# Kernel tuning notes

Hardware: AMD Instinct MI355X
Metric: run time of the kernel (lower is better)

## Reference

```python
import jax, jax.numpy as jnp
import numpy as np

B, M, D, H, DH = 8, 1024, 768, 12, 64
R, RF, RW, DFF = 32, 384, 384, 3072
EPS = 1e-12  # BERT LayerNorm eps


def _ln(z, g, b):
    mu = jnp.mean(z, -1, keepdims=True)
    var = jnp.mean((z - mu) ** 2, -1, keepdims=True)
    return g * (z - mu) * jax.lax.rsqrt(var + EPS) + b


def setup_inputs() -> dict:
    ks = jax.random.split(jax.random.key(0), 20)
    n = lambda k, s: jax.random.normal(k, s, dtype=jnp.float32) * 0.02
    return {
        "x": jax.random.normal(ks[0], (B, M, D), dtype=jnp.float32),
        "mask": jnp.zeros((B, M), jnp.float32),  # additive attention mask
        "Pq": n(ks[1], (H, D, R)), "Vq": n(ks[2], (H, R, DH)), "bq": n(ks[3], (H, DH)),
        "Pk": n(ks[4], (H, D, R)), "Vk": n(ks[5], (H, R, DH)), "bk": n(ks[6], (H, DH)),
        "Pv": n(ks[7], (H, D, R)), "Vv": n(ks[8], (H, R, DH)), "bv": n(ks[9], (H, DH)),
        "Uo": n(ks[10], (D, RW)), "Vo": n(ks[11], (RW, D)), "bo_attn": n(ks[12], (D,)),
        "U1": n(ks[13], (D, RF)), "V1": n(ks[14], (RF, DFF)), "b1": n(ks[15], (DFF,)),
        "U2": n(ks[16], (DFF, RF)), "V2": n(ks[17], (RF, D)), "b2": n(ks[18], (D,)),
        "ln1_g": jnp.ones((D,), jnp.float32), "ln1_b": jnp.zeros((D,), jnp.float32),
        "ln2_g": jnp.ones((D,), jnp.float32), "ln2_b": jnp.zeros((D,), jnp.float32),
    }


def reference(x, mask, Pq, Vq, bq, Pk, Vk, bk, Pv, Vv, bv, Uo, Vo, bo_attn,
              U1, V1, b1, U2, V2, b2, ln1_g, ln1_b, ln2_g, ln2_b):
    Bx, Mx, dm = x.shape
    dh = dm // Pq.shape[0]
    scale = 1.0 / (dh ** 0.5)
    # low-rank per-head Q/K/V: x @ P (d->r) then @ V (r->dh), + per-head bias
    Q = jnp.einsum('bmd,hdr,hrk->bhmk', x, Pq, Vq) + bq[None, :, None, :]
    K = jnp.einsum('bmd,hdr,hrk->bhmk', x, Pk, Vk) + bk[None, :, None, :]
    V = jnp.einsum('bmd,hdr,hrk->bhmk', x, Pv, Vv) + bv[None, :, None, :]
    scores = jnp.einsum('bhmk,bhnk->bhmn', Q, K) * scale + mask[:, None, None, :]
    probs = jax.nn.softmax(scores, axis=-1)
    attn = jnp.einsum('bhmn,bhnk->bhmk', probs, V)
    attn = attn.transpose(0, 2, 1, 3).reshape(Bx, Mx, dm)  # (B, M, d_model)
    # low-rank attention output projection + residual + LN1
    x1 = _ln(x + (attn @ Uo) @ Vo + bo_attn, ln1_g, ln1_b)
    # low-rank FFN: GELU((x1 @ U1) @ V1 + b1) @ U2 @ V2 + b2 (BERT exact gelu)
    mid = x1 @ U1
    y = (jax.nn.gelu(mid @ V1 + b1, approximate=False) @ U2) @ V2 + b2
    return _ln(x1 + y, ln2_g, ln2_b)
```

## Files before the change

### kernel.cpp

```cpp
#include <hip/hip_runtime.h>
#include <cstddef>

#define D_MODEL 768
#define NHEAD   12
#define DHEAD   64
#define RANK    32
#define SEQ     1024
#define BATCH   8
#define BM      8192

typedef __attribute__((ext_vector_type(8))) short short8;
typedef __attribute__((ext_vector_type(4))) float floatx4;

__device__ inline ushort f2b(float f) {
  union { float f; unsigned u; } v; v.f = f;
  unsigned r = v.u + 0x7fffu + ((v.u >> 16) & 1u);
  return (ushort)(r >> 16);
}
__device__ inline float b2f(ushort h) {
  union { unsigned u; float f; } v; v.u = ((unsigned)h) << 16;
  return v.f;
}
__device__ inline unsigned pk2(float a, float b) {
  return ((__float_as_uint(b) + 0x8000u) & 0xffff0000u) |
         ((__float_as_uint(a) + 0x8000u) >> 16);
}
__device__ inline float fast_gelu(float x) {
  float z = 0.79788456080286536f * (x + 0.044715f * x * x * x);
  float e = __expf(2.f * z);
  float t = 1.f - 2.f / (e + 1.f);
  return 0.5f * x * (1.f + t);
}

__global__ __launch_bounds__(256) void f2b_kernel(
    const float* __restrict__ in, ushort* __restrict__ out, int n) {
  int i = (blockIdx.x * 256 + threadIdx.x) * 4;
  if (i >= n) return;
  float4 v = *(const float4*)(in + i);
  ushort4 o;
  o.x = f2b(v.x); o.y = f2b(v.y); o.z = f2b(v.z); o.w = f2b(v.w);
  *(ushort4*)(out + i) = o;
}

__global__ __launch_bounds__(256) void combine_qkv_kernel(
    const float* __restrict__ Pq, const float* __restrict__ Vq,
    const float* __restrict__ Pk, const float* __restrict__ Vk,
    const float* __restrict__ Pv, const float* __restrict__ Vv,
    ushort* __restrict__ Wt) {
  int which = blockIdx.y;
  const float* P  = which == 0 ? Pq : (which == 1 ? Pk : Pv);
  const float* Vw = which == 0 ? Vq : (which == 1 ? Vk : Vv);
  ushort* W = Wt + (size_t)which * D_MODEL * D_MODEL;
  int idx = blockIdx.x * 256 + threadIdx.x;
  if (idx >= D_MODEL * NHEAD * DHEAD) return;
  int c = idx / D_MODEL;
  int d = idx - c * D_MODEL;
  int h = c >> 6, k = c & 63;
  const float* p = P + ((size_t)h * D_MODEL + d) * RANK;
  const float* v = Vw + (size_t)h * RANK * DHEAD + k;
  float s = 0.f;
#pragma unroll
  for (int r = 0; r < RANK; r++) s += p[r] * v[(size_t)r * DHEAD];
  W[(size_t)c * D_MODEL + d] = f2b(s);
}

__global__ __launch_bounds__(256) void concat_bias_kernel(
    const float* __restrict__ bq, const float* __restrict__ bk,
    const float* __restrict__ bv, float* __restrict__ out) {
  int i = blockIdx.x * 256 + threadIdx.x;
  if (i >= 2304) return;
  out[i] = (i < 768) ? bq[i] : (i < 1536 ? bk[i - 768] : bv[i - 1536]);
}

__global__ __launch_bounds__(256) void prep_weights_kernel(
    const float* __restrict__ U1, const float* __restrict__ V1,
    const float* __restrict__ U2, const float* __restrict__ V2,
    const float* __restrict__ Vo, const float* __restrict__ Uo,
    ushort* __restrict__ U1t, ushort* __restrict__ V1t,
    ushort* __restrict__ U2t, ushort* __restrict__ V2t,
    ushort* __restrict__ VoT, ushort* __restrict__ Uob) {
  __shared__ float t[32][33];
  int blk = blockIdx.x;
  if (blk >= 3168) {
    int i = (blk - 3168) * 1024 + threadIdx.x * 4;
    float4 v = *(const float4*)(Uo + i);
    ushort4 o;
    o.x = f2b(v.x); o.y = f2b(v.y); o.z = f2b(v.z); o.w = f2b(v.w);
    *(ushort4*)(Uob + i) = o;
    return;
  }
  const float* in; ushort* out; int R, C, bx, by;
  if (blk < 288)       { in = U1; out = U1t; R = 768;  C = 384;  int i = blk;        bx = i % 12; by = i / 12; }
  else if (blk < 1440) { in = V1; out = V1t; R = 384;  C = 3072; int i = blk - 288;  bx = i % 96; by = i / 96; }
  else if (blk < 2592) { in = U2; out = U2t; R = 3072; C = 384;  int i = blk - 1440; bx = i % 12; by = i / 12; }
  else if (blk < 2880) { in = V2; out = V2t; R = 384;  C = 768;  int i = blk - 2592; bx = i % 24; by = i / 24; }
  else                 { in = Vo; out = VoT; R = 384;  C = 768;  int i = blk - 2880; bx = i % 24; by = i / 24; }
  int c0 = bx * 32, r0 = by * 32;
  int lx = threadIdx.x & 31, ly = threadIdx.x >> 5;
#pragma unroll
  for (int i = 0; i < 32; i += 8)
    t[ly + i][lx] = in[(size_t)(r0 + ly + i) * C + c0 + lx];
  __syncthreads();
#pragma unroll
  for (int i = 0; i < 32; i += 8)
    out[(size_t)(c0 + ly + i) * R + r0 + lx] = f2b(t[lx][ly + i]);
}

template <int OUTMODE, int BIAS, int GELU>
__global__ __launch_bounds__(256, 2) void gemm_mfma_kernel(
    const ushort* __restrict__ A, const ushort* __restrict__ Bt,
    const float* __restrict__ bias, void* __restrict__ C,
    void* __restrict__ C2, void* __restrict__ C3,
    int M, int N, int K) {
  __shared__ __align__(16) ushort Als[2][128 * 64];
  __shared__ __align__(16) ushort Bls[2][128 * 64];
  const int tid  = threadIdx.x;
  const int lane = tid & 63;
  const int quad = lane >> 4, l16 = lane & 15;
  const int wu   = __builtin_amdgcn_readfirstlane(tid >> 6);
  const int wrow = (wu >> 1) * 64, wcol = (wu & 1) * 64;
  const int row0 = blockIdx.x * 128, col0 = blockIdx.y * 128;

  const int r_ = tid >> 3, sl_ = tid & 7;
  const ushort* Ag = A + (size_t)(row0 + r_) * K + sl_ * 8;
  const ushort* Bg = Bt + (size_t)(col0 + r_) * K + sl_ * 8;
  const int loff = r_ * 64 + ((sl_ ^ (r_ & 7)) << 3);

  const int nsteps = K >> 6;
  short8 ast[4], bst[4];

#pragma unroll
  for (int p = 0; p < 4; p++) {
    ast[p] = *(const short8*)(Ag + (size_t)(32 * p) * K);
    bst[p] = *(const short8*)(Bg + (size_t)(32 * p) * K);
  }
#pragma unroll
  for (int p = 0; p < 4; p++) {
    *(short8*)(&Als[0][0] + loff + p * (32 * 64)) = ast[p];
    *(short8*)(&Bls[0][0] + loff + p * (32 * 64)) = bst[p];
  }
#pragma unroll
  for (int p = 0; p < 4; p++) {
    ast[p] = *(const short8*)(Ag + (size_t)(32 * p) * K + 64);
    bst[p] = *(const short8*)(Bg + (size_t)(32 * p) * K + 64);
  }
  asm volatile("s_waitcnt lgkmcnt(0)" ::: "memory");
  __builtin_amdgcn_s_barrier();
  asm volatile("" ::: "memory");

  floatx4 acc[4][4] = {};

  for (int s = 0; s < nsteps; s++) {
    const int cur = s & 1;

    if (s + 1 < nsteps) {
#pragma unroll
      for (int p = 0; p < 4; p++) {
        *(short8*)(&Als[cur ^ 1][0] + loff + p * (32 * 64)) = ast[p];
        *(short8*)(&Bls[cur ^ 1][0] + loff + p * (32 * 64)) = bst[p];
      }
      if (s + 2 < nsteps) {
        const int ko = (s + 2) * 64;
#pragma unroll
        for (int p = 0; p < 4; p++) {
          ast[p] = *(const short8*)(Ag + (size_t)(32 * p) * K + ko);
          bst[p] = *(const short8*)(Bg + (size_t)(32 * p) * K + ko);
        }
      }
    }

    __builtin_amdgcn_s_setprio(1);
#pragma unroll
    for (int kk = 0; kk < 2; kk++) {
      short8 af[4], bf[4];
#pragma unroll
      for (int mt = 0; mt < 4; mt++) {
        int row = wrow + mt * 16 + l16;
        af[mt] = *(const short8*)(&Als[cur][0] + row * 64
                                  + (((kk * 4 + quad) ^ (l16 & 7)) << 3));
      }
#pragma unroll
      for (int nt = 0; nt < 4; nt++) {
        int row = wcol + nt * 16 + l16;
        bf[nt] = *(const short8*)(&Bls[cur][0] + row * 64
                                  + (((kk * 4 + quad) ^ (l16 & 7)) << 3));
      }
#pragma unroll
      for (int mt = 0; mt < 4; mt++)
#pragma unroll
        for (int nt = 0; nt < 4; nt++)
          acc[mt][nt] = __builtin_amdgcn_mfma_f32_16x16x32_bf16(
              af[mt], bf[nt], acc[mt][nt], 0, 0, 0);
    }
    __builtin_amdgcn_s_setprio(0);

    if (s + 1 < nsteps) {
      asm volatile("s_waitcnt lgkmcnt(0)" ::: "memory");
      __builtin_amdgcn_s_barrier();
      asm volatile("" ::: "memory");
    }
  }

#pragma unroll
  for (int mt = 0; mt < 4; mt++) {
#pragma unroll
    for (int nt = 0; nt < 4; nt++) {
      int colg = col0 + wcol + nt * 16 + l16;
      float bv_ = BIAS ? bias[colg] : 0.f;
      float v4[4];
#pragma unroll
      for (int r = 0; r < 4; r++) {
        float v = acc[mt][nt][r] + bv_;
        if (GELU) v = fast_gelu(v);
        v4[r] = v;
      }
      int rowg0 = row0 + wrow + mt * 16 + quad * 4;
      if (OUTMODE == 3) {
        int seg = col0 / 768;
        int cl = colg - seg * 768;
        if (seg == 2) {
          ushort4 o;
          o.x = f2b(v4[0]); o.y = f2b(v4[1]); o.z = f2b(v4[2]); o.w = f2b(v4[3]);
          *(ushort4*)((ushort*)C3 + (size_t)cl * BM + rowg0) = o;
        } else {
          ushort* dst = (seg == 0) ? (ushort*)C : (ushort*)C2;
          float sc = (seg == 0) ? 0.125f : 1.f;
#pragma unroll
          for (int r = 0; r < 4; r++)
            dst[(size_t)(rowg0 + r) * D_MODEL + cl] = f2b(v4[r] * sc);
        }
      } else {
#pragma unroll
        for (int r = 0; r < 4; r++)
          ((ushort*)C)[(size_t)(rowg0 + r) * N + colg] = f2b(v4[r]);
      }
    }
  }
}

template <int BIAS>
__global__ __launch_bounds__(256) void gemm_n64_kernel(
    const ushort* __restrict__ A, const ushort* __restrict__ Bt,
    const float* __restrict__ bias, ushort* __restrict__ C,
    int M, int N, int K) {
  __shared__ __align__(16) ushort Als[128 * 32];
  __shared__ __align__(16) ushort Bls[64 * 32];
  const int tid  = threadIdx.x;
  const int lane = tid & 63;
  const int quad = lane >> 4, l16 = lane & 15;
  const int wu   = __builtin_amdgcn_readfirstlane(tid >> 6);
  const int row0 = blockIdx.x * 128, col0 = blockIdx.y * 64;

  floatx4 acc[2][4] = {};

  for (int k0 = 0; k0 < K; k0 += 32) {
    __syncthreads();
#pragma unroll
    for (int is = 0; is < 2; is++) {
      int c = is * 256 + wu * 64 + lane;
      int m = c >> 2, kk = (c & 3) << 3;
      const ushort* ga = A + (size_t)(row0 + m) * K + (k0 + kk);
      ushort* la = Als + (size_t)(is * 256 + wu * 64) * 8;
      __builtin_amdgcn_global_load_lds(
          (const __attribute__((address_space(1))) void*)ga,
          (__attribute__((address_space(3))) void*)la, 16, 0, 0);
    }
    {
      int c = wu * 64 + lane;
      int m = c >> 2, kk = (c & 3) << 3;
      const ushort* gb = Bt + (size_t)(col0 + m) * K + (k0 + kk);
      ushort* lb = Bls + (size_t)(wu * 64) * 8;
      __builtin_amdgcn_global_load_lds(
          (const __attribute__((address_space(1))) void*)gb,
          (__attribute__((address_space(3))) void*)lb, 16, 0, 0);
    }
    __syncthreads();

    short8 af[2], bf[4];
#pragma unroll
    for (int mt = 0; mt < 2; mt++)
      af[mt] = *(const short8*)(Als + ((wu * 32 + mt * 16 + l16) * 32 + quad * 8));
#pragma unroll
    for (int nt = 0; nt < 4; nt++)
      bf[nt] = *(const short8*)(Bls + ((nt * 16 + l16) * 32 + quad * 8));
#pragma unroll
    for (int mt = 0; mt < 2; mt++)
#pragma unroll
      for (int nt = 0; nt < 4; nt++)
        acc[mt][nt] = __builtin_amdgcn_mfma_f32_16x16x32_bf16(
            af[mt], bf[nt], acc[mt][nt], 0, 0, 0);
  }

#pragma unroll
  for (int mt = 0; mt < 2; mt++) {
#pragma unroll
    for (int nt = 0; nt < 4; nt++) {
      int colg = col0 + nt * 16 + l16;
      float bv_ = BIAS ? bias[colg] : 0.f;
      int rowg0 = row0 + wu * 32 + mt * 16 + quad * 4;
#pragma unroll
      for (int r = 0; r < 4; r++)
        C[(size_t)(rowg0 + r) * N + colg] = f2b(acc[mt][nt][r] + bv_);
    }
  }
}

__global__ __launch_bounds__(256) void gemm_mfma_splitk_kernel(
    const ushort* __restrict__ A, const ushort* __restrict__ Bt,
    float* __restrict__ Cpart, int M, int N, int Ktot, int Kper) {
  __shared__ __align__(16) ushort Als[128 * 32];
  __shared__ __align__(16) ushort Bls[128 * 32];
  const int tid  = threadIdx.x;
  const int lane = tid & 63;
  const int quad = lane >> 4, l16 = lane & 15;
  const int wu   = __builtin_amdgcn_readfirstlane(tid >> 6);
  const int wrow = (wu >> 1) * 64, wcol = (wu & 1) * 64;
  const int row0 = blockIdx.x * 128, col0 = blockIdx.y * 128;
  const int kbase = blockIdx.z * Kper;
  float* Cz = Cpart + (size_t)blockIdx.z * M * N;

  floatx4 acc[4][4] = {};

  for (int k0 = kbase; k0 < kbase + Kper; k0 += 32) {
    __syncthreads();
#pragma unroll
    for (int is = 0; is < 2; is++) {
      int c = is * 256 + wu * 64 + lane;
      int m = c >> 2, kk = (c & 3) << 3;
      const ushort* ga = A + (size_t)(row0 + m) * Ktot + (k0 + kk);
      ushort* la = Als + (size_t)(is * 256 + wu * 64) * 8;
      __builtin_amdgcn_global_load_lds(
          (const __attribute__((address_space(1))) void*)ga,
          (__attribute__((address_space(3))) void*)la, 16, 0, 0);
      const ushort* gb = Bt + (size_t)(col0 + m) * Ktot + (k0 + kk);
      ushort* lb = Bls + (size_t)(is * 256 + wu * 64) * 8;
      __builtin_amdgcn_global_load_lds(
          (const __attribute__((address_space(1))) void*)gb,
          (__attribute__((address_space(3))) void*)lb, 16, 0, 0);
    }
    __syncthreads();

    short8 af[4], bf[4];
#pragma unroll
    for (int mt = 0; mt < 4; mt++)
      af[mt] = *(const short8*)(Als + ((wrow + mt * 16 + l16) * 32 + quad * 8));
#pragma unroll
    for (int nt = 0; nt < 4; nt++)
      bf[nt] = *(const short8*)(Bls + ((wcol + nt * 16 + l16) * 32 + quad * 8));
#pragma unroll
    for (int mt = 0; mt < 4; mt++)
#pragma unroll
      for (int nt = 0; nt < 4; nt++)
        acc[mt][nt] = __builtin_amdgcn_mfma_f32_16x16x32_bf16(
            af[mt], bf[nt], acc[mt][nt], 0, 0, 0);
  }

#pragma unroll
  for (int mt = 0; mt < 4; mt++)
#pragma unroll
    for (int nt = 0; nt < 4; nt++) {
      int colg = col0 + wcol + nt * 16 + l16;
      int rowg0 = row0 + wrow + mt * 16 + quad * 4;
#pragma unroll
      for (int r = 0; r < 4; r++)
        Cz[(size_t)(rowg0 + r) * N + colg] = acc[mt][nt][r];
    }
}

__global__ __launch_bounds__(256) void reduce_splitk_kernel(
    const float* __restrict__ part, ushort* __restrict__ out, int n, int S) {
  int i = (blockIdx.x * 256 + threadIdx.x) * 4;
  if (i >= n) return;
  float4 a = *(const float4*)(part + i);
  for (int s = 1; s < S; s++) {
    float4 b = *(const float4*)(part + (size_t)s * n + i);
    a.x += b.x; a.y += b.y; a.z += b.z; a.w += b.w;
  }
  ushort4 o;
  o.x = f2b(a.x); o.y = f2b(a.y); o.z = f2b(a.z); o.w = f2b(a.w);
  *(ushort4*)(out + i) = o;
}

__global__ __launch_bounds__(256, 3) void attn_mfma_kernel(
    const ushort* __restrict__ Q, const ushort* __restrict__ K,
    const ushort* __restrict__ Vt, const float* __restrict__ mask,
    ushort* __restrict__ O) {
  const int bid  = blockIdx.x;
  const int xcd  = bid & 7;
  const int rest = bid >> 3;
  const int qt   = rest & 7;
  const int grp  = (rest >> 3) * 8 + xcd;
  const int h = grp % 12, b = grp / 12;

  const int tid = threadIdx.x;
  const int lane = tid & 63;
  const int quad = lane >> 4, l16 = lane & 15;
  const int wu = __builtin_amdgcn_readfirstlane(tid >> 6);
  const int qrow0 = qt * 128 + wu * 32;

  __shared__ __align__(16) ushort Ks[2][64 * 64];
  __shared__ __align__(16) ushort Vts[2][64 * 64];
  __shared__ __align__(16) float Msk[SEQ];

  *(float4*)(Msk + tid * 4) = *(const float4*)(mask + (size_t)b * SEQ + tid * 4);

  short8 qf[2][2];
#pragma unroll
  for (int rt = 0; rt < 2; rt++) {
    const ushort* qp = Q + ((size_t)(b * SEQ + qrow0 + rt * 16 + l16)) * D_MODEL
                     + h * DHEAD + quad * 8;
    qf[rt][0] = *(const short8*)qp;
    qf[rt][1] = *(const short8*)(qp + 32);
  }

  const int j0 = tid >> 3, ck = tid & 7;
  const ushort* Kg = K + ((size_t)(b * SEQ + j0)) * D_MODEL + h * DHEAD + ck * 8;
  const ushort* Vg = Vt + ((size_t)(h * DHEAD + j0)) * BM + b * SEQ + ck * 8;
  const int kloff = j0 * 64 + ((ck ^ (j0 & 7)) << 3);

  short8 kst[2], vst[2];
#pragma unroll
  for (int p = 0; p < 2; p++) {
    kst[p] = *(const short8*)(Kg + (size_t)(p * 32) * D_MODEL);
    vst[p] = *(const short8*)(Vg + (size_t)p * (32 * BM));
  }
#pragma unroll
  for (int p = 0; p < 2; p++) {
    *(short8*)(&Ks[0][0] + kloff + p * (32 * 64)) = kst[p];
    *(short8*)(&Vts[0][0] + kloff + p * (32 * 64)) = vst[p];
  }
#pragma unroll
  for (int p = 0; p < 2; p++) {
    kst[p] = *(const short8*)(Kg + (size_t)(64 + p * 32) * D_MODEL);
    vst[p] = *(const short8*)(Vg + 64 + (size_t)p * (32 * BM));
  }
  asm volatile("s_waitcnt lgkmcnt(0)" ::: "memory");
  __builtin_amdgcn_s_barrier();
  asm volatile("" ::: "memory");

  float lsum[2] = {0.f, 0.f};
  floatx4 o_acc[2][4] = {};

  for (int n0 = 0; n0 < SEQ; n0 += 64) {
    const int cur = (n0 >> 6) & 1;

    if (n0 + 64 < SEQ) {
#pragma unroll
      for (int p = 0; p < 2; p++) {
        *(short8*)(&Ks[cur ^ 1][0] + kloff + p * (32 * 64)) = kst[p];
        *(short8*)(&Vts[cur ^ 1][0] + kloff + p * (32 * 64)) = vst[p];
      }
      if (n0 + 128 < SEQ) {
#pragma unroll
        for (int p = 0; p < 2; p++) {
          kst[p] = *(const short8*)(Kg + (size_t)(n0 + 128 + p * 32) * D_MODEL);
          vst[p] = *(const short8*)(Vg + (n0 + 128) + (size_t)p * (32 * BM));
        }
      }
    }

    __builtin_amdgcn_s_setprio(1);
    unsigned UA[2][4], UB[2][4];
#pragma unroll
    for (int ct = 0; ct < 4; ct++) {
      int krow = ct * 16 + l16;
      int sa = (quad ^ (l16 & 7)) << 3;
      const ushort* kbp = &Ks[cur][0] + krow * 64;
      short8 ka = *(const short8*)(kbp + sa);
      short8 kb = *(const short8*)(kbp + (sa ^ 32));
      float4 mk = *(const float4*)(Msk + n0 + ct * 16 + quad * 4);
#pragma unroll
      for (int rt = 0; rt < 2; rt++) {
        floatx4 st = {};
        st = __builtin_amdgcn_mfma_f32_16x16x32_bf16(ka, qf[rt][0], st, 0, 0, 0);
        st = __builtin_amdgcn_mfma_f32_16x16x32_bf16(kb, qf[rt][1], st, 0, 0, 0);
        float e0 = __expf(st[0] + mk.x);
        float e1 = __expf(st[1] + mk.y);
        float e2 = __expf(st[2] + mk.z);
        float e3 = __expf(st[3] + mk.w);
        lsum[rt] += (e0 + e1) + (e2 + e3);
        UA[rt][ct] = pk2(e0, e1);
        UB[rt][ct] = pk2(e2, e3);
      }
    }

#pragma unroll
    for (int kk = 0; kk < 2; kk++) {
      short8 pa[2];
#pragma unroll
      for (int rt = 0; rt < 2; rt++) {
        unsigned a0 = UA[rt][2 * kk], a2 = UA[rt][2 * kk + 1];
        unsigned b1 = UB[rt][2 * kk], b3 = UB[rt][2 * kk + 1];
        asm("v_permlane32_swap_b32 %0, %1" : "+v"(a0), "+v"(a2));
        asm("v_permlane16_swap_b32 %0, %1" : "+v"(a0), "+v"(a2));
        asm("v_permlane32_swap_b32 %0, %1" : "+v"(b1), "+v"(b3));
        asm("v_permlane16_swap_b32 %0, %1" : "+v"(b1), "+v"(b3));
        int4 t;
        t.x = (int)a0;
        t.y = (int)b1;
        t.z = (int)a2;
        t.w = (int)b3;
        pa[rt] = *(short8*)&t;
      }
#pragma unroll
      for (int dt = 0; dt < 4; dt++) {
        int vr = dt * 16 + l16;
        short8 vb = *(const short8*)(&Vts[cur][0] + vr * 64
                                     + (((kk * 4 + quad) ^ (l16 & 7)) << 3));
#pragma unroll
        for (int rt = 0; rt < 2; rt++)
          o_acc[rt][dt] = __builtin_amdgcn_mfma_f32_16x16x32_bf16(
              pa[rt], vb, o_acc[rt][dt], 0, 0, 0);
      }
    }
    __builtin_amdgcn_s_setprio(0);

    if (n0 + 64 < SEQ) {
      asm volatile("s_waitcnt lgkmcnt(0)" ::: "memory");
      __builtin_amdgcn_s_barrier();
      asm volatile("" ::: "memory");
    }
  }

#pragma unroll
  for (int rt = 0; rt < 2; rt++) {
    float l = lsum[rt];
    l += __shfl_xor(l, 16);
    l += __shfl_xor(l, 32);
    float inv = 1.f / l;
    int lanebase = lane & 48;
#pragma unroll
    for (int rr = 0; rr < 4; rr++) {
      int iv = __builtin_amdgcn_ds_bpermute((lanebase | (quad * 4 + rr)) << 2,
                                            __float_as_int(inv));
      float invr = __int_as_float(iv);
      size_t rowg = (size_t)(b * SEQ + qrow0 + rt * 16 + quad * 4 + rr);
#pragma unroll
      for (int dt = 0; dt < 4; dt++)
        O[rowg * D_MODEL + h * DHEAD + dt * 16 + l16] = f2b(o_acc[rt][dt][rr] * invr);
    }
  }
}

template <int AIN_BF16, int OUT_FP32, int OUT_BF16>
__global__ __launch_bounds__(256) void add_ln_kernel(
    const float* __restrict__ Ainf, const ushort* __restrict__ Ainb,
    const ushort* __restrict__ Binb,
    const float* __restrict__ g, const float* __restrict__ bt,
    float* __restrict__ outf, ushort* __restrict__ outb) {
  const int row = blockIdx.x, tid = threadIdx.x;
  __shared__ float red[4];
  float v[3];
  float s = 0.f;
#pragma unroll
  for (int u = 0; u < 3; u++) {
    int c = tid + u * 256;
    float a = AIN_BF16 ? b2f(Ainb[(size_t)row * 768 + c]) : Ainf[(size_t)row * 768 + c];
    v[u] = a + b2f(Binb[(size_t)row * 768 + c]);
    s += v[u];
  }
#pragma unroll
  for (int off = 32; off > 0; off >>= 1) s += __shfl_down(s, off);
  if ((tid & 63) == 0) red[tid >> 6] = s;
  __syncthreads();
  float mu = (red[0] + red[1] + red[2] + red[3]) * (1.f / 768.f);
  float s2 = 0.f;
#pragma unroll
  for (int u = 0; u < 3; u++) { float d = v[u] - mu; s2 += d * d; }
#pragma unroll
  for (int off = 32; off > 0; off >>= 1) s2 += __shfl_down(s2, off);
  __syncthreads();
  if ((tid & 63) == 0) red[tid >> 6] = s2;
  __syncthreads();
  float var = (red[0] + red[1] + red[2] + red[3]) * (1.f / 768.f);
  float inv = rsqrtf(var + 1e-12f);
#pragma unroll
  for (int u = 0; u < 3; u++) {
    int c = tid + u * 256;
    float r = g[c] * (v[u] - mu) * inv + bt[c];
    if (OUT_FP32) outf[(size_t)row * 768 + c] = r;
    if (OUT_BF16) outb[(size_t)row * 768 + c] = f2b(r);
  }
}

extern "C" void kernel_launch(void* const* d_in, const int* in_sizes, int n_in,
                              void* d_out, int out_size, void* d_ws, size_t ws_size,
                              hipStream_t stream) {
  const float* x    = (const float*)d_in[0];
  const float* mask = (const float*)d_in[1];
  const float* Pq   = (const float*)d_in[2];
  const float* Vq   = (const float*)d_in[3];
  const float* bq   = (const float*)d_in[4];
  const float* Pk   = (const float*)d_in[5];
  const float* Vk   = (const float*)d_in[6];
  const float* bk   = (const float*)d_in[7];
  const float* Pv   = (const float*)d_in[8];
  const float* Vv   = (const float*)d_in[9];
  const float* bv   = (const float*)d_in[10];
  const float* Uo   = (const float*)d_in[11];
  const float* Vo   = (const float*)d_in[12];
  const float* bo   = (const float*)d_in[13];
  const float* U1   = (const float*)d_in[14];
  const float* V1   = (const float*)d_in[15];
  const float* b1   = (const float*)d_in[16];
  const float* U2   = (const float*)d_in[17];
  const float* V2   = (const float*)d_in[18];
  const float* b2   = (const float*)d_in[19];
  const float* g1   = (const float*)d_in[20];
  const float* be1  = (const float*)d_in[21];
  const float* g2   = (const float*)d_in[22];
  const float* be2  = (const float*)d_in[23];

  char* w = (char*)d_ws;
  auto alloc = [&](size_t bytes) -> char* {
    char* p = w; w += (bytes + 255) & ~(size_t)255; return p;
  };
  ushort* xb     = (ushort*)alloc((size_t)BM * 768 * 2);
  ushort* Wqkvt  = (ushort*)alloc((size_t)2304 * 768 * 2);
  float*  ball   = (float*)alloc(2304 * 4);
  ushort* VoT    = (ushort*)alloc(768 * 384 * 2);
  ushort* Uob    = (ushort*)alloc(768 * 384 * 2);
  ushort* Wot    = (ushort*)alloc(768 * 768 * 2);
  ushort* U1t    = (ushort*)alloc(384 * 768 * 2);
  ushort* V1t    = (ushort*)alloc((size_t)3072 * 384 * 2);
  ushort* U2t    = (ushort*)alloc((size_t)384 * 3072 * 2);
  ushort* V2t    = (ushort*)alloc(768 * 384 * 2);
  ushort* Qb     = (ushort*)alloc((size_t)BM * 768 * 2);
  ushort* Kb     = (ushort*)alloc((size_t)BM * 768 * 2);
  ushort* Vtb    = (ushort*)alloc((size_t)768 * BM * 2);
  ushort* attnb  = (ushort*)alloc((size_t)BM * 768 * 2);
  ushort* mtb    = (ushort*)alloc((size_t)BM * 384 * 2);
  ushort* y1b    = (ushort*)alloc((size_t)BM * 768 * 2);
  ushort* x1b    = (ushort*)alloc((size_t)BM * 768 * 2);
  float*  part   = (float*)alloc((size_t)4 * BM * 384 * 4);
  ushort* hiddenb = Qb;
  ushort* y2b     = y1b;
  float*  outp    = (float*)d_out;

  f2b_kernel<<<(BM * 768) / 1024, 256, 0, stream>>>(x, xb, BM * 768);
  combine_qkv_kernel<<<dim3(2304, 3), 256, 0, stream>>>(Pq, Vq, Pk, Vk, Pv, Vv, Wqkvt);
  concat_bias_kernel<<<9, 256, 0, stream>>>(bq, bk, bv, ball);
  prep_weights_kernel<<<3456, 256, 0, stream>>>(U1, V1, U2, V2, Vo, Uo,
                                                U1t, V1t, U2t, V2t, VoT, Uob);
  gemm_n64_kernel<0><<<dim3(6, 12), 256, 0, stream>>>(VoT, Uob, nullptr, Wot, 768, 768, 384);

  gemm_mfma_kernel<3, 1, 0><<<dim3(64, 18), 256, 0, stream>>>(
      xb, Wqkvt, ball, Qb, Kb, Vtb, BM, 2304, 768);

  attn_mfma_kernel<<<dim3(768), 256, 0, stream>>>(Qb, Kb, Vtb, mask, attnb);

  gemm_mfma_kernel<1, 1, 0><<<dim3(64, 6), 256, 0, stream>>>(
      attnb, Wot, bo, y1b, nullptr, nullptr, BM, 768, 768);
  add_ln_kernel<0, 0, 1><<<BM, 256, 0, stream>>>(x, nullptr, y1b, g1, be1, nullptr, x1b);

  gemm_mfma_kernel<1, 0, 0><<<dim3(64, 3), 256, 0, stream>>>(
      x1b, U1t, nullptr, mtb, nullptr, nullptr, BM, 384, 768);
  gemm_mfma_kernel<1, 1, 1><<<dim3(64, 24), 256, 0, stream>>>(
      mtb, V1t, b1, hiddenb, nullptr, nullptr, BM, 3072, 384);
  gemm_mfma_splitk_kernel<<<dim3(64, 3, 2), 256, 0, stream>>>(
      hiddenb, U2t, part, BM, 384, 3072, 1536);
  reduce_splitk_kernel<<<(BM * 384) / 1024, 256, 0, stream>>>(part, mtb, BM * 384, 2);
  gemm_mfma_kernel<1, 1, 0><<<dim3(64, 6), 256, 0, stream>>>(
      mtb, V2t, b2, y2b, nullptr, nullptr, BM, 768, 384);

  add_ln_kernel<1, 1, 0><<<BM, 256, 0, stream>>>(nullptr, x1b, y2b, g2, be2, outp, nullptr);
}
```

Baseline: 403.8 us.

## Add 256x256-tile 512-thread MFMA GEMM for QKV and FFN up-projection

Introduces a new GEMM kernel with 256x256 output tiles, 8 waves each computing 128x64, a K-step of 32 and double-buffered LDS with register prefetch. It replaces the 128x128 kernel for the fused QKV projection and the GELU FFN up-projection. The larger tile raises arithmetic intensity and cuts global reloads of A and B. In exchange it launches far fewer blocks (288 and 384), uses more accumulator registers per thread, and synchronises more often because the K-step is shorter, which may hurt occupancy and wave balance across CUs.

```diff
diff --git a/kernel.cpp b/kernel.cpp
--- a/kernel.cpp
+++ b/kernel.cpp
@@ -104,6 +104,130 @@
 #pragma unroll
   for (int i = 0; i < 32; i += 8)
     out[(size_t)(c0 + ly + i) * R + r0 + lx] = f2b(t[lx][ly + i]);
+}
+
+template <int OUTMODE, int BIAS, int GELU>
+__global__ __launch_bounds__(512, 2) void gemm_mfma256_kernel(
+    const ushort* __restrict__ A, const ushort* __restrict__ Bt,
+    const float* __restrict__ bias, void* __restrict__ C,
+    void* __restrict__ C2, void* __restrict__ C3,
+    int M, int N, int K) {
+  __shared__ __align__(16) ushort Als[2][256 * 32];
+  __shared__ __align__(16) ushort Bls[2][256 * 32];
+  const int tid  = threadIdx.x;
+  const int lane = tid & 63;
+  const int quad = lane >> 4, l16 = lane & 15;
+  const int wu   = __builtin_amdgcn_readfirstlane(tid >> 6);
+  const int wrow = (wu >> 2) * 128, wcol = (wu & 3) * 64;
+  const int row0 = blockIdx.x * 256, col0 = blockIdx.y * 256;
+
+  const int r_ = tid >> 2, sl_ = tid & 3;
+  const ushort* Ag = A + (size_t)(row0 + r_) * K + sl_ * 8;
+  const ushort* Bg = Bt + (size_t)(col0 + r_) * K + sl_ * 8;
+  const int loff = r_ * 32 + ((sl_ ^ ((r_ >> 1) & 3)) << 3);
+  const int srd = (quad ^ ((l16 >> 1) & 3)) << 3;
+
+  const int nsteps = K >> 5;
+  short8 ast[2], bst[2];
+
+#pragma unroll
+  for (int p = 0; p < 2; p++) {
+    ast[p] = *(const short8*)(Ag + (size_t)(128 * p) * K);
+    bst[p] = *(const short8*)(Bg + (size_t)(128 * p) * K);
+  }
+#pragma unroll
+  for (int p = 0; p < 2; p++) {
+    *(short8*)(&Als[0][0] + loff + p * (128 * 32)) = ast[p];
+    *(short8*)(&Bls[0][0] + loff + p * (128 * 32)) = bst[p];
+  }
+#pragma unroll
+  for (int p = 0; p < 2; p++) {
+    ast[p] = *(const short8*)(Ag + (size_t)(128 * p) * K + 32);
+    bst[p] = *(const short8*)(Bg + (size_t)(128 * p) * K + 32);
+  }
+  asm volatile("s_waitcnt lgkmcnt(0)" ::: "memory");
+  __builtin_amdgcn_s_barrier();
+  asm volatile("" ::: "memory");
+
+  floatx4 acc[8][4] = {};
+
+  for (int s = 0; s < nsteps; s++) {
+    const int cur = s & 1;
+
+    if (s + 1 < nsteps) {
+#pragma unroll
+      for (int p = 0; p < 2; p++) {
+        *(short8*)(&Als[cur ^ 1][0] + loff + p * (128 * 32)) = ast[p];
+        *(short8*)(&Bls[cur ^ 1][0] + loff + p * (128 * 32)) = bst[p];
+      }
+      if (s + 2 < nsteps) {
+        const int ko = (s + 2) * 32;
+#pragma unroll
+        for (int p = 0; p < 2; p++) {
+          ast[p] = *(const short8*)(Ag + (size_t)(128 * p) * K + ko);
+          bst[p] = *(const short8*)(Bg + (size_t)(128 * p) * K + ko);
+        }
+      }
+    }
+
+    __builtin_amdgcn_s_setprio(1);
+    short8 af[8], bf[4];
+#pragma unroll
+    for (int mt = 0; mt < 8; mt++)
+      af[mt] = *(const short8*)(&Als[cur][0] + (wrow + mt * 16 + l16) * 32 + srd);
+#pragma unroll
+    for (int nt = 0; nt < 4; nt++)
+      bf[nt] = *(const short8*)(&Bls[cur][0] + (wcol + nt * 16 + l16) * 32 + srd);
+#pragma unroll
+    for (int mt = 0; mt < 8; mt++)
+#pragma unroll
+      for (int nt = 0; nt < 4; nt++)
+        acc[mt][nt] = __builtin_amdgcn_mfma_f32_16x16x32_bf16(
+            af[mt], bf[nt], acc[mt][nt], 0, 0, 0);
+    __builtin_amdgcn_s_setprio(0);
+
+    if (s + 1 < nsteps) {
+      asm volatile("s_waitcnt lgkmcnt(0)" ::: "memory");
+      __builtin_amdgcn_s_barrier();
+      asm volatile("" ::: "memory");
+    }
+  }
+
+#pragma unroll
+  for (int mt = 0; mt < 8; mt++) {
+#pragma unroll
+    for (int nt = 0; nt < 4; nt++) {
+      int colg = col0 + wcol + nt * 16 + l16;
+      float bv_ = BIAS ? bias[colg] : 0.f;
+      float v4[4];
+#pragma unroll
+      for (int r = 0; r < 4; r++) {
+        float v = acc[mt][nt][r] + bv_;
+        if (GELU) v = fast_gelu(v);
+        v4[r] = v;
+      }
+      int rowg0 = row0 + wrow + mt * 16 + quad * 4;
+      if (OUTMODE == 3) {
+        int seg = col0 / 768;
+        int cl = colg - seg * 768;
+        if (seg == 2) {
+          ushort4 o;
+          o.x = f2b(v4[0]); o.y = f2b(v4[1]); o.z = f2b(v4[2]); o.w = f2b(v4[3]);
+          *(ushort4*)((ushort*)C3 + (size_t)cl * BM + rowg0) = o;
+        } else {
+          ushort* dst = (seg == 0) ? (ushort*)C : (ushort*)C2;
+          float sc = (seg == 0) ? 0.125f : 1.f;
+#pragma unroll
+          for (int r = 0; r < 4; r++)
+            dst[(size_t)(rowg0 + r) * D_MODEL + cl] = f2b(v4[r] * sc);
+        }
+      } else {
+#pragma unroll
+        for (int r = 0; r < 4; r++)
+          ((ushort*)C)[(size_t)(rowg0 + r) * N + colg] = f2b(v4[r]);
+      }
+    }
+  }
 }
 
 template <int OUTMODE, int BIAS, int GELU>
@@ -644,7 +768,7 @@
                                                 U1t, V1t, U2t, V2t, VoT, Uob);
   gemm_n64_kernel<0><<<dim3(6, 12), 256, 0, stream>>>(VoT, Uob, nullptr, Wot, 768, 768, 384);
 
-  gemm_mfma_kernel<3, 1, 0><<<dim3(64, 18), 256, 0, stream>>>(
+  gemm_mfma256_kernel<3, 1, 0><<<dim3(32, 9), 512, 0, stream>>>(
       xb, Wqkvt, ball, Qb, Kb, Vtb, BM, 2304, 768);
 
   attn_mfma_kernel<<<dim3(768), 256, 0, stream>>>(Qb, Kb, Vtb, mask, attnb);
@@ -655,7 +779,7 @@
 
   gemm_mfma_kernel<1, 0, 0><<<dim3(64, 3), 256, 0, stream>>>(
       x1b, U1t, nullptr, mtb, nullptr, nullptr, BM, 384, 768);
-  gemm_mfma_kernel<1, 1, 1><<<dim3(64, 24), 256, 0, stream>>>(
+  gemm_mfma256_kernel<1, 1, 1><<<dim3(32, 12), 512, 0, stream>>>(
       mtb, V1t, b1, hiddenb, nullptr, nullptr, BM, 3072, 384);
   gemm_mfma_splitk_kernel<<<dim3(64, 3, 2), 256, 0, stream>>>(
       hiddenb, U2t, part, BM, 384, 3072, 1536);
```

After: 423.9 us. +5.0%, slower.

## Fuse fp32-to-bf16 input conversion into QKV GEMM and pipeline split-K GEMM

Applied to the files above, without the earlier changes.

The standalone kernel that converts x to bf16 is removed. The QKV GEMM now reads fp32 x directly and packs it to bf16 while staging into LDS, which saves a kernel launch and a full write/read round trip of the converted activation. The split-K GEMM for the FFN down-projection is replaced by a double-buffered, register-prefetched 64-wide K-step version that matches the main GEMM, instead of the old single-buffer global_load_lds loop with two syncthreads per step. The trade-off is that the QKV A-tile loads double in bytes and need extra registers for the fp32 staging values.

```diff
diff --git a/kernel.cpp b/kernel.cpp
--- a/kernel.cpp
+++ b/kernel.cpp
@@ -30,16 +30,6 @@
   float e = __expf(2.f * z);
   float t = 1.f - 2.f / (e + 1.f);
   return 0.5f * x * (1.f + t);
-}
-
-__global__ __launch_bounds__(256) void f2b_kernel(
-    const float* __restrict__ in, ushort* __restrict__ out, int n) {
-  int i = (blockIdx.x * 256 + threadIdx.x) * 4;
-  if (i >= n) return;
-  float4 v = *(const float4*)(in + i);
-  ushort4 o;
-  o.x = f2b(v.x); o.y = f2b(v.y); o.z = f2b(v.z); o.w = f2b(v.w);
-  *(ushort4*)(out + i) = o;
 }
 
 __global__ __launch_bounds__(256) void combine_qkv_kernel(
@@ -106,7 +96,7 @@
     out[(size_t)(c0 + ly + i) * R + r0 + lx] = f2b(t[lx][ly + i]);
 }
 
-template <int OUTMODE, int BIAS, int GELU>
+template <int OUTMODE, int BIAS, int GELU, int AFP32 = 0>
 __global__ __launch_bounds__(256, 2) void gemm_mfma_kernel(
     const ushort* __restrict__ A, const ushort* __restrict__ Bt,
     const float* __restrict__ bias, void* __restrict__ C,
@@ -123,25 +113,48 @@
 
   const int r_ = tid >> 3, sl_ = tid & 7;
   const ushort* Ag = A + (size_t)(row0 + r_) * K + sl_ * 8;
+  const float*  Agf = (const float*)A + (size_t)(row0 + r_) * K + sl_ * 8;
   const ushort* Bg = Bt + (size_t)(col0 + r_) * K + sl_ * 8;
   const int loff = r_ * 64 + ((sl_ ^ (r_ & 7)) << 3);
 
   const int nsteps = K >> 6;
   short8 ast[4], bst[4];
+  float4 asf[4][2];
+
+  auto loadA = [&](int p, int ko) {
+    if (AFP32) {
+      asf[p][0] = *(const float4*)(Agf + (size_t)(32 * p) * K + ko);
+      asf[p][1] = *(const float4*)(Agf + (size_t)(32 * p) * K + ko + 4);
+    } else {
+      ast[p] = *(const short8*)(Ag + (size_t)(32 * p) * K + ko);
+    }
+  };
+  auto writeA = [&](int buf, int p) {
+    if (AFP32) {
+      int4 t;
+      t.x = (int)pk2(asf[p][0].x, asf[p][0].y);
+      t.y = (int)pk2(asf[p][0].z, asf[p][0].w);
+      t.z = (int)pk2(asf[p][1].x, asf[p][1].y);
+      t.w = (int)pk2(asf[p][1].z, asf[p][1].w);
+      *(short8*)(&Als[buf][0] + loff + p * (32 * 64)) = *(short8*)&t;
+    } else {
+      *(short8*)(&Als[buf][0] + loff + p * (32 * 64)) = ast[p];
+    }
+  };
 
 #pragma unroll
   for (int p = 0; p < 4; p++) {
-    ast[p] = *(const short8*)(Ag + (size_t)(32 * p) * K);
+    loadA(p, 0);
     bst[p] = *(const short8*)(Bg + (size_t)(32 * p) * K);
   }
 #pragma unroll
   for (int p = 0; p < 4; p++) {
-    *(short8*)(&Als[0][0] + loff + p * (32 * 64)) = ast[p];
+    writeA(0, p);
     *(short8*)(&Bls[0][0] + loff + p * (32 * 64)) = bst[p];
   }
 #pragma unroll
   for (int p = 0; p < 4; p++) {
-    ast[p] = *(const short8*)(Ag + (size_t)(32 * p) * K + 64);
+    loadA(p, 64);
     bst[p] = *(const short8*)(Bg + (size_t)(32 * p) * K + 64);
   }
   asm volatile("s_waitcnt lgkmcnt(0)" ::: "memory");
@@ -156,14 +169,14 @@
     if (s + 1 < nsteps) {
 #pragma unroll
       for (int p = 0; p < 4; p++) {
-        *(short8*)(&Als[cur ^ 1][0] + loff + p * (32 * 64)) = ast[p];
+        writeA(cur ^ 1, p);
         *(short8*)(&Bls[cur ^ 1][0] + loff + p * (32 * 64)) = bst[p];
       }
       if (s + 2 < nsteps) {
         const int ko = (s + 2) * 64;
 #pragma unroll
         for (int p = 0; p < 4; p++) {
-          ast[p] = *(const short8*)(Ag + (size_t)(32 * p) * K + ko);
+          loadA(p, ko);
           bst[p] = *(const short8*)(Bg + (size_t)(32 * p) * K + ko);
         }
       }
@@ -236,6 +249,126 @@
       }
     }
   }
+}
+
+__global__ __launch_bounds__(256, 2) void gemm_piped_splitk_kernel(
+    const ushort* __restrict__ A, const ushort* __restrict__ Bt,
+    float* __restrict__ Cpart, int M, int N, int Ktot, int Kper) {
+  __shared__ __align__(16) ushort Als[2][128 * 64];
+  __shared__ __align__(16) ushort Bls[2][128 * 64];
+  const int tid  = threadIdx.x;
+  const int lane = tid & 63;
+  const int quad = lane >> 4, l16 = lane & 15;
+  const int wu   = __builtin_amdgcn_readfirstlane(tid >> 6);
+  const int wrow = (wu >> 1) * 64, wcol = (wu & 1) * 64;
+  const int row0 = blockIdx.x * 128, col0 = blockIdx.y * 128;
+  const int kbase = blockIdx.z * Kper;
+  float* Cz = Cpart + (size_t)blockIdx.z * M * N;
+
+  const int r_ = tid >> 3, sl_ = tid & 7;
+  const ushort* Ag = A + (size_t)(row0 + r_) * Ktot + kbase + sl_ * 8;
+  const ushort* Bg = Bt + (size_t)(col0 + r_) * Ktot + kbase + sl_ * 8;
+  const int loff = r_ * 64 + ((sl_ ^ (r_ & 7)) << 3);
+
+  const int nsteps = Kper >> 6;
+  short8 ast[4], bst[4];
+
+#pragma unroll
+  for (int p = 0; p < 4; p++) {
+    ast[p] = *(const short8*)(Ag + (size_t)(32 * p) * Ktot);
+    bst[p] = *(const short8*)(Bg + (size_t)(32 * p) * Ktot);
+  }
+#pragma unroll
+  for (int p = 0; p < 4; p++) {
+    *(short8*)(&Als[0][0] + loff + p * (32 * 64)) = ast[p];
+    *(short8*)(&Bls[0][0] + loff + p * (32 * 64)) = bst[p];
+  }
+#pragma unroll
+  for (int p = 0; p < 4; p++) {
+    ast[p] = *(const short8*)(Ag + (size_t)(32 * p) * Ktot + 64);
+    bst[p] = *(const short8*)(Bg + (size_t)(32 * p) * Ktot + 64);
+  }
+  asm volatile("s_waitcnt lgkmcnt(0)" ::: "memory");
+  __builtin_amdgcn_s_barrier();
+  asm volatile("" ::: "memory");
+
+  floatx4 acc[4][4] = {};
+
+  for (int s = 0; s < nsteps; s++) {
+    const int cur = s & 1;
+
+    if (s + 1 < nsteps) {
+#pragma unroll
+      for (int p = 0; p < 4; p++) {
+        *(short8*)(&Als[cur ^ 1][0] + loff + p * (32 * 64)) = ast[p];
+        *(short8*)(&Bls[cur ^ 1][0] + loff + p * (32 * 64)) = bst[p];
+      }
+      if (s + 2 < nsteps) {
+        const int ko = (s + 2) * 64;
+#pragma unroll
+        for (int p = 0; p < 4; p++) {
+          ast[p] = *(const short8*)(Ag + (size_t)(32 * p) * Ktot + ko);
+          bst[p] = *(const short8*)(Bg + (size_t)(32 * p) * Ktot + ko);
+        }
+      }
+    }
+
+    __builtin_amdgcn_s_setprio(1);
+#pragma unroll
+    for (int kk = 0; kk < 2; kk++) {
+      short8 af[4], bf[4];
+#pragma unroll
+      for (int mt = 0; mt < 4; mt++) {
+        int row = wrow + mt * 16 + l16;
+        af[mt] = *(const short8*)(&Als[cur][0] + row * 64
+                                  + (((kk * 4 + quad) ^ (l16 & 7)) << 3));
+      }
+#pragma unroll
+      for (int nt = 0; nt < 4; nt++) {
+        int row = wcol + nt * 16 + l16;
+        bf[nt] = *(const short8*)(&Bls[cur][0] + row * 64
+                                  + (((kk * 4 + quad) ^ (l16 & 7)) << 3));
+      }
+#pragma unroll
+      for (int mt = 0; mt < 4; mt++)
+#pragma unroll
+        for (int nt = 0; nt < 4; nt++)
+          acc[mt][nt] = __builtin_amdgcn_mfma_f32_16x16x32_bf16(
+              af[mt], bf[nt], acc[mt][nt], 0, 0, 0);
+    }
+    __builtin_amdgcn_s_setprio(0);
+
+    if (s + 1 < nsteps) {
+      asm volatile("s_waitcnt lgkmcnt(0)" ::: "memory");
+      __builtin_amdgcn_s_barrier();
+      asm volatile("" ::: "memory");
+    }
+  }
+
+#pragma unroll
+  for (int mt = 0; mt < 4; mt++)
+#pragma unroll
+    for (int nt = 0; nt < 4; nt++) {
+      int colg = col0 + wcol + nt * 16 + l16;
+      int rowg0 = row0 + wrow + mt * 16 + quad * 4;
+#pragma unroll
+      for (int r = 0; r < 4; r++)
+        Cz[(size_t)(rowg0 + r) * N + colg] = acc[mt][nt][r];
+    }
+}
+
+__global__ __launch_bounds__(256) void reduce_splitk_kernel(
+    const float* __restrict__ part, ushort* __restrict__ out, int n, int S) {
+  int i = (blockIdx.x * 256 + threadIdx.x) * 4;
+  if (i >= n) return;
+  float4 a = *(const float4*)(part + i);
+  for (int s = 1; s < S; s++) {
+    float4 b = *(const float4*)(part + (size_t)s * n + i);
+    a.x += b.x; a.y += b.y; a.z += b.z; a.w += b.w;
+  }
+  ushort4 o;
+  o.x = f2b(a.x); o.y = f2b(a.y); o.z = f2b(a.z); o.w = f2b(a.w);
+  *(ushort4*)(out + i) = o;
 }
 
 template <int BIAS>
@@ -303,82 +436,6 @@
         C[(size_t)(rowg0 + r) * N + colg] = f2b(acc[mt][nt][r] + bv_);
     }
   }
-}
-
-__global__ __launch_bounds__(256) void gemm_mfma_splitk_kernel(
-    const ushort* __restrict__ A, const ushort* __restrict__ Bt,
-    float* __restrict__ Cpart, int M, int N, int Ktot, int Kper) {
-  __shared__ __align__(16) ushort Als[128 * 32];
-  __shared__ __align__(16) ushort Bls[128 * 32];
-  const int tid  = threadIdx.x;
-  const int lane = tid & 63;
-  const int quad = lane >> 4, l16 = lane & 15;
-  const int wu   = __builtin_amdgcn_readfirstlane(tid >> 6);
-  const int wrow = (wu >> 1) * 64, wcol = (wu & 1) * 64;
-  const int row0 = blockIdx.x * 128, col0 = blockIdx.y * 128;
-  const int kbase = blockIdx.z * Kper;
-  float* Cz = Cpart + (size_t)blockIdx.z * M * N;
-
-  floatx4 acc[4][4] = {};
-
-  for (int k0 = kbase; k0 < kbase + Kper; k0 += 32) {
-    __syncthreads();
-#pragma unroll
-    for (int is = 0; is < 2; is++) {
-      int c = is * 256 + wu * 64 + lane;
-      int m = c >> 2, kk = (c & 3) << 3;
-      const ushort* ga = A + (size_t)(row0 + m) * Ktot + (k0 + kk);
-      ushort* la = Als + (size_t)(is * 256 + wu * 64) * 8;
-      __builtin_amdgcn_global_load_lds(
-          (const __attribute__((address_space(1))) void*)ga,
-          (__attribute__((address_space(3))) void*)la, 16, 0, 0);
-      const ushort* gb = Bt + (size_t)(col0 + m) * Ktot + (k0 + kk);
-      ushort* lb = Bls + (size_t)(is * 256 + wu * 64) * 8;
-      __builtin_amdgcn_global_load_lds(
-          (const __attribute__((address_space(1))) void*)gb,
-          (__attribute__((address_space(3))) void*)lb, 16, 0, 0);
-    }
-    __syncthreads();
-
-    short8 af[4], bf[4];
-#pragma unroll
-    for (int mt = 0; mt < 4; mt++)
-      af[mt] = *(const short8*)(Als + ((wrow + mt * 16 + l16) * 32 + quad * 8));
-#pragma unroll
-    for (int nt = 0; nt < 4; nt++)
-      bf[nt] = *(const short8*)(Bls + ((wcol + nt * 16 + l16) * 32 + quad * 8));
-#pragma unroll
-    for (int mt = 0; mt < 4; mt++)
-#pragma unroll
-      for (int nt = 0; nt < 4; nt++)
-        acc[mt][nt] = __builtin_amdgcn_mfma_f32_16x16x32_bf16(
-            af[mt], bf[nt], acc[mt][nt], 0, 0, 0);
-  }
-
-#pragma unroll
-  for (int mt = 0; mt < 4; mt++)
-#pragma unroll
-    for (int nt = 0; nt < 4; nt++) {
-      int colg = col0 + wcol + nt * 16 + l16;
-      int rowg0 = row0 + wrow + mt * 16 + quad * 4;
-#pragma unroll
-      for (int r = 0; r < 4; r++)
-        Cz[(size_t)(rowg0 + r) * N + colg] = acc[mt][nt][r];
-    }
-}
-
-__global__ __launch_bounds__(256) void reduce_splitk_kernel(
-    const float* __restrict__ part, ushort* __restrict__ out, int n, int S) {
-  int i = (blockIdx.x * 256 + threadIdx.x) * 4;
-  if (i >= n) return;
-  float4 a = *(const float4*)(part + i);
-  for (int s = 1; s < S; s++) {
-    float4 b = *(const float4*)(part + (size_t)s * n + i);
-    a.x += b.x; a.y += b.y; a.z += b.z; a.w += b.w;
-  }
-  ushort4 o;
-  o.x = f2b(a.x); o.y = f2b(a.y); o.z = f2b(a.z); o.w = f2b(a.w);
-  *(ushort4*)(out + i) = o;
 }
 
 __global__ __launch_bounds__(256, 3) void attn_mfma_kernel(
@@ -615,7 +672,6 @@
   auto alloc = [&](size_t bytes) -> char* {
     char* p = w; w += (bytes + 255) & ~(size_t)255; return p;
   };
-  ushort* xb     = (ushort*)alloc((size_t)BM * 768 * 2);
   ushort* Wqkvt  = (ushort*)alloc((size_t)2304 * 768 * 2);
   float*  ball   = (float*)alloc(2304 * 4);
   ushort* VoT    = (ushort*)alloc(768 * 384 * 2);
@@ -637,15 +693,14 @@
   ushort* y2b     = y1b;
   float*  outp    = (float*)d_out;
 
-  f2b_kernel<<<(BM * 768) / 1024, 256, 0, stream>>>(x, xb, BM * 768);
   combine_qkv_kernel<<<dim3(2304, 3), 256, 0, stream>>>(Pq, Vq, Pk, Vk, Pv, Vv, Wqkvt);
   concat_bias_kernel<<<9, 256, 0, stream>>>(bq, bk, bv, ball);
   prep_weights_kernel<<<3456, 256, 0, stream>>>(U1, V1, U2, V2, Vo, Uo,
                                                 U1t, V1t, U2t, V2t, VoT, Uob);
   gemm_n64_kernel<0><<<dim3(6, 12), 256, 0, stream>>>(VoT, Uob, nullptr, Wot, 768, 768, 384);
 
-  gemm_mfma_kernel<3, 1, 0><<<dim3(64, 18), 256, 0, stream>>>(
-      xb, Wqkvt, ball, Qb, Kb, Vtb, BM, 2304, 768);
+  gemm_mfma_kernel<3, 1, 0, 1><<<dim3(64, 18), 256, 0, stream>>>(
+      (const ushort*)x, Wqkvt, ball, Qb, Kb, Vtb, BM, 2304, 768);
 
   attn_mfma_kernel<<<dim3(768), 256, 0, stream>>>(Qb, Kb, Vtb, mask, attnb);
 
@@ -657,7 +712,7 @@
       x1b, U1t, nullptr, mtb, nullptr, nullptr, BM, 384, 768);
   gemm_mfma_kernel<1, 1, 1><<<dim3(64, 24), 256, 0, stream>>>(
       mtb, V1t, b1, hiddenb, nullptr, nullptr, BM, 3072, 384);
-  gemm_mfma_splitk_kernel<<<dim3(64, 3, 2), 256, 0, stream>>>(
+  gemm_piped_splitk_kernel<<<dim3(64, 3, 2), 256, 0, stream>>>(
       hiddenb, U2t, part, BM, 384, 3072, 1536);
   reduce_splitk_kernel<<<(BM * 384) / 1024, 256, 0, stream>>>(part, mtb, BM * 384, 2);
   gemm_mfma_kernel<1, 1, 0><<<dim3(64, 6), 256, 0, stream>>>(
```

Result: faster. 389.3 us (-3.6%).
